# Optimization experiments

Hardware: AMD Instinct MI355X
Metric: run time of the kernel (lower is better)

## Reference

```python
import jax, jax.numpy as jnp
import numpy as np

EPS = 1e-5  # GraphNorm eps


def setup_inputs() -> dict:
    key = jax.random.key(0)
    ks = jax.random.split(key, 8)
    B, N, D, L = 8, 2048, 128, 3
    return {
        "instance": jax.random.uniform(ks[0], (B, N, 2), jnp.float32),
        "Wn": jax.random.normal(ks[1], (D, 2), jnp.float32) * 0.5,
        "bn": jnp.zeros((D,), jnp.float32),
        "Wg": jax.random.normal(ks[2], (L, D, D), jnp.float32) / np.sqrt(D).astype(np.float32),
        "bg": jnp.zeros((L, D), jnp.float32),
        "gn_w": jnp.ones((D,), jnp.float32),
        "gn_b": jnp.zeros((D,), jnp.float32),
        "gn_a": jnp.ones((D,), jnp.float32),
    }


def reference(instance, Wn, bn, Wg, bg, gn_w, gn_b, gn_a):
    # instance: [B, N, 2] city coordinates. Graph is complete, so the PyG
    # edge-list GCN over all (i != j) pairs + self-loops is exactly a dense
    # symmetric-normalized adjacency matmul per graph.
    B, N, _ = instance.shape
    # pairwise Euclidean distances (cdist), safe sqrt to keep diagonal exact 0
    sq = jnp.sum(instance * instance, axis=-1)                      # [B, N]
    d2 = sq[:, :, None] + sq[:, None, :] - 2.0 * jnp.einsum(
        'bnd,bmd->bnm', instance, instance)                          # [B, N, N]
    pos = d2 > 0
    dist = jnp.where(pos, jnp.sqrt(jnp.where(pos, d2, 1.0)), 0.0)    # [B, N, N]
    # GCN edge weights = distances, self-loops added with weight 1.0
    A = dist + jnp.eye(N, dtype=dist.dtype)
    deg = jnp.sum(A, axis=-1)                                        # [B, N]
    dinv = jax.lax.rsqrt(deg)
    An = dinv[:, :, None] * A * dinv[:, None, :]                     # D^-1/2 A D^-1/2

    h = jnp.einsum('bne,de->bnd', instance, Wn) + bn                 # proj_node
    for l in range(Wg.shape[0]):
        # GCNConv: aggregate normalized messages of lin(x), then bias
        hw = jnp.einsum('bnm,bmd->bnd', An, jnp.einsum('bnd,ed->bne', h, Wg[l])) + bg[l]
        h = jnp.tanh(hw) + h                                         # activation + residual
        # GraphNorm (shared params across layers): per-graph, per-feature stats
        mean = jnp.mean(h, axis=1, keepdims=True)                    # [B, 1, D]
        sub = h - gn_a * mean
        var = jnp.mean(sub * sub, axis=1, keepdims=True)
        h = gn_w * sub * jax.lax.rsqrt(var + EPS) + gn_b
    return h  # [B, N, D] (unbatch+stack of equal-size graphs)
```

## Files before the change

### kernel.cpp

```cpp
#include <hip/hip_runtime.h>
#include <hip/hip_bf16.h>
#include <math.h>

#define BB 8
#define NN 2048
#define DD 128
#define LL 3
#define GN_EPS 1e-5f

typedef __attribute__((ext_vector_type(8))) short bf16x8;
typedef __attribute__((ext_vector_type(4))) float f32x4;
typedef __attribute__((ext_vector_type(8))) unsigned short u16x8;

#define FSQRT(x) __builtin_amdgcn_sqrtf(x)

__device__ __forceinline__ unsigned short f2bf(float f) {
    union { float f; unsigned u; } v; v.f = f;
    return (unsigned short)((v.u + 0x8000u) >> 16);
}

__device__ __forceinline__ float fast_tanh(float x) {
    float e = __expf(-2.0f * fabsf(x));
    float t = (1.0f - e) * __builtin_amdgcn_rcpf(1.0f + e);
    return copysignf(t, x);
}

__device__ __forceinline__ void stats_sc(float ps, float pq, float a, float w_,
                                         float b_, float& s, float& c) {
    const float inv_n = 1.0f / (float)NN;
    float mean = ps * inv_n;
    float msq  = pq * inv_n;
    float var  = msq - mean * mean * a * (2.0f - a);
    float rstd = rsqrtf(var + GN_EPS);
    s = w_ * rstd;
    c = b_ - s * (a * mean);
}


__global__ __launch_bounds__(256)
void prep_wg(const float* __restrict__ Wg, const float* __restrict__ Wn,
             const float* __restrict__ bn, unsigned short* __restrict__ wgf,
             float* __restrict__ weff, float* __restrict__ beff)
{
    const int f = blockIdx.x * 256 + threadIdx.x;
    const int l  = f >> 14;
    const int r  = f & 16383;
    const int dp = r >> 7;
    const int e  = r & 127;
    const int dpt = dp >> 4, ll = dp & 15;
    const int kc  = e >> 5,  eo = e & 31;
    wgf[((((l * 8 + dpt) * 4 + kc) * 16 + ll) << 5) + eo] = f2bf(Wg[f]);

    if (blockIdx.x == 0 && threadIdx.x < 128) {
        const int ee = threadIdx.x;
        float a0 = 0.f, a1 = 0.f, cc = 0.f;
        for (int d = 0; d < 128; ++d) {
            const float wv = Wg[ee * 128 + d];
            a0 = fmaf(wv, Wn[d * 2 + 0], a0);
            a1 = fmaf(wv, Wn[d * 2 + 1], a1);
            cc = fmaf(wv, bn[d], cc);
        }
        weff[ee * 2 + 0] = a0;
        weff[ee * 2 + 1] = a1;
        beff[ee] = cc;
    }
}

__global__ __launch_bounds__(256)
void gen_pack(const float* __restrict__ inst, const float* __restrict__ Wn,
              const float* __restrict__ bn, const float* __restrict__ weff,
              const float* __restrict__ beff,
              float* __restrict__ dinv, float* __restrict__ h,
              unsigned short* __restrict__ tp,
              float* __restrict__ psum, float* __restrict__ psq)
{
    __shared__ float cs[NN * 2];
    __shared__ float part[4][16];
    const int b     = blockIdx.x & 7;
    const int ntile = blockIdx.x >> 3;
    const int n0    = ntile * 16;
    const int tid   = threadIdx.x;
    const int w     = tid >> 6;
    const int lane  = tid & 63;
    const int lq    = lane >> 4;
    const int ll    = lane & 15;

    const float* instb = inst + b * NN * 2;
    for (int i = tid; i < (NN * 2) / 4; i += 256)
        ((float4*)cs)[i] = ((const float4*)instb)[i];
    __syncthreads();

    const int n = n0 + ll;
    const float nx = cs[n * 2 + 0];
    const float ny = cs[n * 2 + 1];

    const int diagkcg = ntile >> 1;
    float rs = 0.f;
    for (int kc = 0; kc < 16; ++kc) {
        const int kcg = w * 16 + kc;
        const int mb  = kcg * 32 + lq * 8;
        const float* cp = &cs[mb * 2];
        float4 c01 = *(const float4*)(cp + 0);
        float4 c23 = *(const float4*)(cp + 4);
        float4 c45 = *(const float4*)(cp + 8);
        float4 c67 = *(const float4*)(cp + 12);
        float mxx[8] = { c01.x, c01.z, c23.x, c23.z, c45.x, c45.z, c67.x, c67.z };
        float myy[8] = { c01.y, c01.w, c23.y, c23.w, c45.y, c45.w, c67.y, c67.w };
        float dist[8];
        #pragma unroll
        for (int j = 0; j < 8; ++j) {
            float dx = nx - mxx[j];
            float dy = ny - myy[j];
            dist[j] = FSQRT(dx * dx + dy * dy);
        }
        if (kcg == diagkcg) {
            #pragma unroll
            for (int j = 0; j < 8; ++j)
                if (mb + j == n) dist[j] = 1.0f;
        }
        #pragma unroll
        for (int j = 0; j < 8; ++j) rs += dist[j];
    }

    rs += __shfl_xor(rs, 16);
    rs += __shfl_xor(rs, 32);
    if (lq == 0) part[w][ll] = rs;
    __syncthreads();
    if (tid < 16)
        dinv[b * NN + n0 + tid] = rsqrtf(part[0][tid] + part[1][tid] +
                                         part[2][tid] + part[3][tid]);

    {
        const int d  = tid & 127;
        const int r0 = tid >> 7;
        const float w0 = Wn[d * 2 + 0];
        const float w1 = Wn[d * 2 + 1];
        const float bv = bn[d];
        const float we0 = weff[d * 2 + 0];
        const float we1 = weff[d * 2 + 1];
        const float be  = beff[d];
        const int kcg   = ntile >> 1;
        const int mbase = (ntile & 1) * 16;
        const int dt    = d >> 4;
        const int lld   = d & 15;
        unsigned short* tpd =
            tp + (((size_t)(b * 64 + kcg) * 8 + dt) * 64 + lld) * 8;
        #pragma unroll
        for (int r = r0; r < 16; r += 2) {
            const float x0 = cs[(n0 + r) * 2 + 0];
            const float x1 = cs[(n0 + r) * 2 + 1];
            h[((size_t)b * NN + n0 + r) * DD + d] = fmaf(x0, w0, fmaf(x1, w1, bv));
            const float dv = rsqrtf(part[0][r] + part[1][r] + part[2][r] + part[3][r]);
            const int mloc = mbase + r;
            const int lqa  = mloc >> 3;
            const int j    = mloc & 7;
            tpd[(size_t)lqa * 128 + j] = f2bf(dv * fmaf(x0, we0, fmaf(x1, we1, be)));
        }
    }
    if (blockIdx.x == 0) {
        for (int i = tid; i < LL * BB * DD; i += 256) { psum[i] = 0.f; psq[i] = 0.f; }
    }
}

template <bool HP>
__global__ __launch_bounds__(256)
void lin_mfma(const float* __restrict__ h, const unsigned short* __restrict__ wgf_l,
              const float* __restrict__ dinv,
              const float* __restrict__ psumP, const float* __restrict__ psqP,
              const float* __restrict__ ga, const float* __restrict__ gw,
              const float* __restrict__ gb, unsigned short* __restrict__ tp)
{
    __shared__ float sL[DD], cL[DD];
    const int tid  = threadIdx.x;
    const int b    = blockIdx.x & 7;
    const int tile = blockIdx.x >> 3;
    const int row0 = b * NN + tile * 32;
    const int w    = tid >> 6;
    const int lane = tid & 63;
    const int lq   = lane >> 4;
    const int ll   = lane & 15;

    if (tid < DD) {
        float s = 1.0f, c = 0.0f;
        if (HP)
            stats_sc(psumP[b * DD + tid], psqP[b * DD + tid],
                     ga[tid], gw[tid], gb[tid], s, c);
        sL[tid] = s; cL[tid] = c;
    }
    __syncthreads();

    bf16x8 aw[2][4];
    #pragma unroll
    for (int mt = 0; mt < 2; ++mt) {
        const int dpt = 2 * w + mt;
        #pragma unroll
        for (int kc = 0; kc < 4; ++kc)
            aw[mt][kc] = *(const bf16x8*)&wgf_l[(((dpt * 4 + kc) * 16 + ll) << 5) + lq * 8];
    }

    bf16x8 bh[2][4];
    #pragma unroll
    for (int nt = 0; nt < 2; ++nt) {
        const float* hrow = h + (size_t)(row0 + nt * 16 + ll) * DD;
        #pragma unroll
        for (int kc = 0; kc < 4; ++kc) {
            float4 h0 = *(const float4*)&hrow[kc * 32 + lq * 8];
            float4 h1 = *(const float4*)&hrow[kc * 32 + lq * 8 + 4];
            const int e0 = kc * 32 + lq * 8;
            bf16x8 p;
            p[0] = (short)f2bf(fmaf(sL[e0 + 0], h0.x, cL[e0 + 0]));
            p[1] = (short)f2bf(fmaf(sL[e0 + 1], h0.y, cL[e0 + 1]));
            p[2] = (short)f2bf(fmaf(sL[e0 + 2], h0.z, cL[e0 + 2]));
            p[3] = (short)f2bf(fmaf(sL[e0 + 3], h0.w, cL[e0 + 3]));
            p[4] = (short)f2bf(fmaf(sL[e0 + 4], h1.x, cL[e0 + 4]));
            p[5] = (short)f2bf(fmaf(sL[e0 + 5], h1.y, cL[e0 + 5]));
            p[6] = (short)f2bf(fmaf(sL[e0 + 6], h1.z, cL[e0 + 6]));
            p[7] = (short)f2bf(fmaf(sL[e0 + 7], h1.w, cL[e0 + 7]));
            bh[nt][kc] = p;
        }
    }

    f32x4 acc[2][2];
    #pragma unroll
    for (int i = 0; i < 2; ++i)
        #pragma unroll
        for (int j = 0; j < 2; ++j) acc[i][j] = (f32x4)0.0f;

    #pragma unroll
    for (int kc = 0; kc < 4; ++kc)
        #pragma unroll
        for (int nt = 0; nt < 2; ++nt)
            #pragma unroll
            for (int mt = 0; mt < 2; ++mt)
                acc[nt][mt] = __builtin_amdgcn_mfma_f32_16x16x32_bf16(
                    bh[nt][kc], aw[mt][kc], acc[nt][mt], 0, 0, 0);

    #pragma unroll
    for (int nt = 0; nt < 2; ++nt) {
        const int mloc0 = nt * 16 + lq * 4;
        const int lq_a  = mloc0 >> 3;
        const int j0    = mloc0 & 7;
        float4 di4 = *(const float4*)&dinv[row0 + mloc0];
        #pragma unroll
        for (int mt = 0; mt < 2; ++mt) {
            const int dt = 2 * w + mt;
            ushort4 pk;
            pk.x = f2bf(acc[nt][mt][0] * di4.x);
            pk.y = f2bf(acc[nt][mt][1] * di4.y);
            pk.z = f2bf(acc[nt][mt][2] * di4.z);
            pk.w = f2bf(acc[nt][mt][3] * di4.w);
            *(ushort4*)&tp[((size_t)((b * 64 + tile) * 8 + dt) * 64 + lq_a * 16 + ll) * 8 + j0] = pk;
        }
    }
}

template <bool HP>
__global__ __launch_bounds__(256, 2)
void agg_mfma(const float* __restrict__ inst, const unsigned short* __restrict__ tp,
              const float* __restrict__ dinv, const float* __restrict__ bg_l,
              const float* __restrict__ psumP, const float* __restrict__ psqP,
              const float* __restrict__ ga, const float* __restrict__ gw,
              const float* __restrict__ gb,
              float* __restrict__ h, float* __restrict__ psum, float* __restrict__ psq)
{
    __shared__ float cs[NN * 2];
    __shared__ __align__(16) char plane[2][32768];
    const int b    = blockIdx.x & 7;
    const int t2   = blockIdx.x >> 3;
    const int n0   = t2 * 32;
    const int tid  = threadIdx.x;
    const int w    = tid >> 6;
    const int lane = tid & 63;
    const int lq   = lane >> 4;
    const int ll   = lane & 15;

    const float* instb = inst + b * NN * 2;
    for (int i = tid; i < (NN * 2) / 4; i += 256)
        ((float4*)cs)[i] = ((const float4*)instb)[i];

    const unsigned short* tpb = tp + ((size_t)b * 64 * 8) * 512 + lane * 8;

    f32x4 acc[2][2];
    acc[0][0] = (f32x4)0.0f; acc[0][1] = (f32x4)0.0f;
    acc[1][0] = (f32x4)0.0f; acc[1][1] = (f32x4)0.0f;

    bf16x8 fbA0[4], fbA1[4], fbB0[4], fbB1[4];

    __syncthreads();

    const int   nr0 = n0 + ll;
    const int   nr1 = n0 + 16 + ll;
    const float nx0 = cs[nr0 * 2 + 0], ny0 = cs[nr0 * 2 + 1];
    const float nx1 = cs[nr1 * 2 + 0], ny1 = cs[nr1 * 2 + 1];

#define LOADB_INTO(B0, B1, KK) { \
        _Pragma("unroll") \
        for (int s_ = 0; s_ < 4; ++s_) { \
            B0[s_] = *(const bf16x8*)(tpb + (size_t)(((KK) * 4 + s_) * 8 + 2 * w + 0) * 512); \
            B1[s_] = *(const bf16x8*)(tpb + (size_t)(((KK) * 4 + s_) * 8 + 2 * w + 1) * 512); \
        } \
    }

#define GENQ(PL, PH, Q) { \
        const int kcg_ = (PH) * 16 + w * 4 + (Q); \
        const int mb_  = kcg_ * 32 + lq * 8; \
        const float* cp_ = &cs[mb_ * 2]; \
        float4 c01 = *(const float4*)(cp_ + 0); \
        float4 c23 = *(const float4*)(cp_ + 4); \
        float4 c45 = *(const float4*)(cp_ + 8); \
        float4 c67 = *(const float4*)(cp_ + 12); \
        float mxx[8] = { c01.x, c01.z, c23.x, c23.z, c45.x, c45.z, c67.x, c67.z }; \
        float myy[8] = { c01.y, c01.w, c23.y, c23.w, c45.y, c45.w, c67.y, c67.w }; \
        float dv0[8], dv1[8]; \
        _Pragma("unroll") \
        for (int j = 0; j < 8; ++j) { \
            float dx0 = nx0 - mxx[j], dy0 = ny0 - myy[j]; \
            dv0[j] = FSQRT(dx0 * dx0 + dy0 * dy0); \
            float dx1 = nx1 - mxx[j], dy1 = ny1 - myy[j]; \
            dv1[j] = FSQRT(dx1 * dx1 + dy1 * dy1); \
        } \
        if (kcg_ == t2) {    \
            _Pragma("unroll") \
            for (int j = 0; j < 8; ++j) { \
                if (mb_ + j == nr0) dv0[j] = 1.0f; \
                if (mb_ + j == nr1) dv1[j] = 1.0f; \
            } \
        } \
        u16x8 pk0, pk1; \
        _Pragma("unroll") \
        for (int j = 0; j < 8; ++j) { pk0[j] = f2bf(dv0[j]); pk1[j] = f2bf(dv1[j]); } \
        *(u16x8*)(plane[PL] + (w * 8 + 0 + (Q)) * 1024 + lane * 16) = pk0; \
        *(u16x8*)(plane[PL] + (w * 8 + 4 + (Q)) * 1024 + lane * 16) = pk1; \
    }

#define STEP(PL, I, C0, C1, DOLOAD, N0, N1, KN) { \
        bf16x8 af[2][4]; \
        _Pragma("unroll") \
        for (int nt = 0; nt < 2; ++nt) \
            _Pragma("unroll") \
            for (int s = 0; s < 4; ++s) \
                af[nt][s] = *(const bf16x8*)(plane[PL] + (((I) * 8 + nt * 4 + s) * 1024) + lane * 16); \
        if (DOLOAD) LOADB_INTO(N0, N1, KN) \
        _Pragma("unroll") \
        for (int s = 0; s < 4; ++s) \
            _Pragma("unroll") \
            for (int nt = 0; nt < 2; ++nt) { \
                acc[nt][0] = __builtin_amdgcn_mfma_f32_16x16x32_bf16(C0[s], af[nt][s], acc[nt][0], 0, 0, 0); \
                acc[nt][1] = __builtin_amdgcn_mfma_f32_16x16x32_bf16(C1[s], af[nt][s], acc[nt][1], 0, 0, 0); \
            } \
    }

    GENQ(0, 0, 0) GENQ(0, 0, 1) GENQ(0, 0, 2) GENQ(0, 0, 3)
    LOADB_INTO(fbA0, fbA1, 0)
    __syncthreads();

    STEP(0, 0, fbA0, fbA1, true, fbB0, fbB1, 1)   GENQ(1, 1, 0)
    STEP(0, 1, fbB0, fbB1, true, fbA0, fbA1, 2)   GENQ(1, 1, 1)
    STEP(0, 2, fbA0, fbA1, true, fbB0, fbB1, 3)   GENQ(1, 1, 2)
    STEP(0, 3, fbB0, fbB1, true, fbA0, fbA1, 4)   GENQ(1, 1, 3)
    __syncthreads();

    STEP(1, 0, fbA0, fbA1, true, fbB0, fbB1, 5)   GENQ(0, 2, 0)
    STEP(1, 1, fbB0, fbB1, true, fbA0, fbA1, 6)   GENQ(0, 2, 1)
    STEP(1, 2, fbA0, fbA1, true, fbB0, fbB1, 7)   GENQ(0, 2, 2)
    STEP(1, 3, fbB0, fbB1, true, fbA0, fbA1, 8)   GENQ(0, 2, 3)
    __syncthreads();

    STEP(0, 0, fbA0, fbA1, true, fbB0, fbB1, 9)   GENQ(1, 3, 0)
    STEP(0, 1, fbB0, fbB1, true, fbA0, fbA1, 10)  GENQ(1, 3, 1)
    STEP(0, 2, fbA0, fbA1, true, fbB0, fbB1, 11)  GENQ(1, 3, 2)
    STEP(0, 3, fbB0, fbB1, true, fbA0, fbA1, 12)  GENQ(1, 3, 3)
    __syncthreads();

    STEP(1, 0, fbA0, fbA1, true,  fbB0, fbB1, 13)
    STEP(1, 1, fbB0, fbB1, true,  fbA0, fbA1, 14)
    STEP(1, 2, fbA0, fbA1, true,  fbB0, fbB1, 15)
    STEP(1, 3, fbB0, fbB1, false, fbA0, fbA1, 0)

#undef STEP
#undef GENQ
#undef LOADB_INTO

    const float di0 = dinv[b * NN + n0 + ll];
    const float di1 = dinv[b * NN + n0 + 16 + ll];
    #pragma unroll
    for (int dtl = 0; dtl < 2; ++dtl) {
        const int d0 = (2 * w + dtl) * 16 + lq * 4;
        float4 bg4 = *(const float4*)&bg_l[d0];
        float sres[4] = {1.f, 1.f, 1.f, 1.f}, cres[4] = {0.f, 0.f, 0.f, 0.f};
        if (HP) {
            float4 ps4 = *(const float4*)&psumP[b * DD + d0];
            float4 pq4 = *(const float4*)&psqP[b * DD + d0];
            float4 ga4 = *(const float4*)&ga[d0];
            float4 gw4 = *(const float4*)&gw[d0];
            float4 gb4 = *(const float4*)&gb[d0];
            stats_sc(ps4.x, pq4.x, ga4.x, gw4.x, gb4.x, sres[0], cres[0]);
            stats_sc(ps4.y, pq4.y, ga4.y, gw4.y, gb4.y, sres[1], cres[1]);
            stats_sc(ps4.z, pq4.z, ga4.z, gw4.z, gb4.z, sres[2], cres[2]);
            stats_sc(ps4.w, pq4.w, ga4.w, gw4.w, gb4.w, sres[3], cres[3]);
        }
        float hs[4] = {0.f, 0.f, 0.f, 0.f}, hq[4] = {0.f, 0.f, 0.f, 0.f};
        #pragma unroll
        for (int nt = 0; nt < 2; ++nt) {
            const int n = n0 + nt * 16 + ll;
            const float di = nt ? di1 : di0;
            size_t idx = ((size_t)b * NN + n) * DD + d0;
            float4 hv = *(const float4*)&h[idx];
            float outv[4];
            #pragma unroll
            for (int r = 0; r < 4; ++r) {
                float pre = di * acc[nt][dtl][r] + (&bg4.x)[r];
                outv[r] = fast_tanh(pre) + fmaf(sres[r], (&hv.x)[r], cres[r]);
                hs[r] += outv[r];
                hq[r] += outv[r] * outv[r];
            }
            float4 ov = { outv[0], outv[1], outv[2], outv[3] };
            *(float4*)&h[idx] = ov;
        }

        #pragma unroll
        for (int off = 1; off < 16; off <<= 1) {
            #pragma unroll
            for (int r = 0; r < 4; ++r) {
                hs[r] += __shfl_xor(hs[r], off);
                hq[r] += __shfl_xor(hq[r], off);
            }
        }
        if (ll == 0) {
            #pragma unroll
            for (int r = 0; r < 4; ++r) {
                atomicAdd(&psum[b * DD + d0 + r], hs[r]);
                atomicAdd(&psq[b * DD + d0 + r], hq[r]);
            }
        }
    }
}

__global__ __launch_bounds__(256)
void apply_kernel(const float* __restrict__ h,
                  const float* __restrict__ psum2, const float* __restrict__ psq2,
                  const float* __restrict__ ga, const float* __restrict__ gw,
                  const float* __restrict__ gb, float* __restrict__ dst)
{
    const int i4 = blockIdx.x * 256 + threadIdx.x;
    const int dg = (i4 & 31) * 4;
    const int b  = i4 >> 16;
    float4 hv = ((const float4*)h)[i4];
    float o[4];
    #pragma unroll
    for (int j = 0; j < 4; ++j) {
        const int d = dg + j;
        float s, c;
        stats_sc(psum2[b * DD + d], psq2[b * DD + d], ga[d], gw[d], gb[d], s, c);
        o[j] = fmaf(s, (&hv.x)[j], c);
    }
    float4 ov = { o[0], o[1], o[2], o[3] };
    ((float4*)dst)[i4] = ov;
}

extern "C" void kernel_launch(void* const* d_in, const int* in_sizes, int n_in,
                              void* d_out, int out_size, void* d_ws, size_t ws_size,
                              hipStream_t stream)
{
    const float* inst = (const float*)d_in[0];
    const float* Wn   = (const float*)d_in[1];
    const float* bn   = (const float*)d_in[2];
    const float* Wg   = (const float*)d_in[3];
    const float* bg   = (const float*)d_in[4];
    const float* gw   = (const float*)d_in[5];
    const float* gb   = (const float*)d_in[6];
    const float* ga   = (const float*)d_in[7];
    float* out = (float*)d_out;

    float* ws   = (float*)d_ws;
    float* dinv = ws;
    float* h    = dinv + BB * NN;
    float* psum = h + (size_t)BB * NN * DD;
    float* psq  = psum + LL * BB * DD;
    float* weff = psq + LL * BB * DD;
    float* beff = weff + 2 * DD;
    unsigned short* wgf = (unsigned short*)(beff + DD);
    unsigned short* tp  = wgf + LL * DD * DD;

    prep_wg<<<(LL * DD * DD) / 256, 256, 0, stream>>>(Wg, Wn, bn, wgf, weff, beff);
    gen_pack<<<1024, 256, 0, stream>>>(inst, Wn, bn, weff, beff, dinv, h, tp, psum, psq);

    agg_mfma<false><<<512, 256, 0, stream>>>(
        inst, tp, dinv, bg + 0 * DD, nullptr, nullptr, ga, gw, gb, h, psum, psq);

    for (int l = 1; l < LL; ++l) {
        const unsigned short* wgl = wgf + (size_t)l * DD * DD;
        const float* psP = psum + (size_t)(l - 1) * BB * DD;
        const float* pqP = psq  + (size_t)(l - 1) * BB * DD;
        float* psL = psum + (size_t)l * BB * DD;
        float* pqL = psq  + (size_t)l * BB * DD;
        lin_mfma<true><<<(BB * NN) / 32, 256, 0, stream>>>(
            h, wgl, dinv, psP, pqP, ga, gw, gb, tp);
        agg_mfma<true><<<512, 256, 0, stream>>>(
            inst, tp, dinv, bg + l * DD, psP, pqP, ga, gw, gb, h, psL, pqL);
    }
    apply_kernel<<<(BB * NN * DD / 4) / 256, 256, 0, stream>>>(
        h, psum + 2 * BB * DD, psq + 2 * BB * DD, ga, gw, gb, out);
}
```

Before: 176.4 us.

## Split K across waves in aggregation kernel with LDS cross-wave reduction

The aggregation kernel previously had each wave own two output D-tiles over the full K range. Distance tiles were shared between waves through double-buffered LDS planes with barriers. Now each wave takes a quarter of the K range for all eight D-tiles. It computes its distance fragments directly in registers and never exchanges them through LDS, which removes the per-phase barriers. The partial accumulators are then reduced across waves through a 64KB LDS buffer. In exchange each wave recomputes no distances but needs 16 accumulator vectors plus 16 B-fragment registers, so register pressure rises and occupancy under launch_bounds(256,2) may suffer.

```diff
diff --git a/kernel.cpp b/kernel.cpp
--- a/kernel.cpp
+++ b/kernel.cpp
@@ -264,7 +264,7 @@
               float* __restrict__ h, float* __restrict__ psum, float* __restrict__ psq)
 {
     __shared__ float cs[NN * 2];
-    __shared__ __align__(16) char plane[2][32768];
+    __shared__ __align__(16) char red[65536];
     const int b    = blockIdx.x & 7;
     const int t2   = blockIdx.x >> 3;
     const int n0   = t2 * 32;
@@ -280,11 +280,13 @@
 
     const unsigned short* tpb = tp + ((size_t)b * 64 * 8) * 512 + lane * 8;
 
-    f32x4 acc[2][2];
-    acc[0][0] = (f32x4)0.0f; acc[0][1] = (f32x4)0.0f;
-    acc[1][0] = (f32x4)0.0f; acc[1][1] = (f32x4)0.0f;
-
-    bf16x8 fbA0[4], fbA1[4], fbB0[4], fbB1[4];
+    f32x4 acc[2][8];
+    #pragma unroll
+    for (int nt = 0; nt < 2; ++nt)
+        #pragma unroll
+        for (int dt = 0; dt < 8; ++dt) acc[nt][dt] = (f32x4)0.0f;
+
+    bf16x8 fbE[8], fbO[8];
 
     __syncthreads();
 
@@ -293,16 +295,16 @@
     const float nx0 = cs[nr0 * 2 + 0], ny0 = cs[nr0 * 2 + 1];
     const float nx1 = cs[nr1 * 2 + 0], ny1 = cs[nr1 * 2 + 1];
 
-#define LOADB_INTO(B0, B1, KK) { \
+    const int kcg0 = w * 16;
+
+#define LOADB(DST, KCG) { \
         _Pragma("unroll") \
-        for (int s_ = 0; s_ < 4; ++s_) { \
-            B0[s_] = *(const bf16x8*)(tpb + (size_t)(((KK) * 4 + s_) * 8 + 2 * w + 0) * 512); \
-            B1[s_] = *(const bf16x8*)(tpb + (size_t)(((KK) * 4 + s_) * 8 + 2 * w + 1) * 512); \
-        } \
-    }
-
-#define GENQ(PL, PH, Q) { \
-        const int kcg_ = (PH) * 16 + w * 4 + (Q); \
+        for (int dt_ = 0; dt_ < 8; ++dt_) \
+            DST[dt_] = *(const bf16x8*)(tpb + (size_t)((KCG) * 8 + dt_) * 512); \
+    }
+
+#define STEPK(KC, CUR, NXT, DOLOAD) { \
+        const int kcg_ = kcg0 + (KC); \
         const int mb_  = kcg_ * 32 + lq * 8; \
         const float* cp_ = &cs[mb_ * 2]; \
         float4 c01 = *(const float4*)(cp_ + 0); \
@@ -326,60 +328,60 @@
                 if (mb_ + j == nr1) dv1[j] = 1.0f; \
             } \
         } \
-        u16x8 pk0, pk1; \
+        bf16x8 af0, af1; \
         _Pragma("unroll") \
-        for (int j = 0; j < 8; ++j) { pk0[j] = f2bf(dv0[j]); pk1[j] = f2bf(dv1[j]); } \
-        *(u16x8*)(plane[PL] + (w * 8 + 0 + (Q)) * 1024 + lane * 16) = pk0; \
-        *(u16x8*)(plane[PL] + (w * 8 + 4 + (Q)) * 1024 + lane * 16) = pk1; \
-    }
-
-#define STEP(PL, I, C0, C1, DOLOAD, N0, N1, KN) { \
-        bf16x8 af[2][4]; \
+        for (int j = 0; j < 8; ++j) { \
+            af0[j] = (short)f2bf(dv0[j]); \
+            af1[j] = (short)f2bf(dv1[j]); \
+        } \
+        if (DOLOAD) LOADB(NXT, kcg_ + 1) \
         _Pragma("unroll") \
-        for (int nt = 0; nt < 2; ++nt) \
-            _Pragma("unroll") \
-            for (int s = 0; s < 4; ++s) \
-                af[nt][s] = *(const bf16x8*)(plane[PL] + (((I) * 8 + nt * 4 + s) * 1024) + lane * 16); \
-        if (DOLOAD) LOADB_INTO(N0, N1, KN) \
-        _Pragma("unroll") \
-        for (int s = 0; s < 4; ++s) \
-            _Pragma("unroll") \
-            for (int nt = 0; nt < 2; ++nt) { \
-                acc[nt][0] = __builtin_amdgcn_mfma_f32_16x16x32_bf16(C0[s], af[nt][s], acc[nt][0], 0, 0, 0); \
-                acc[nt][1] = __builtin_amdgcn_mfma_f32_16x16x32_bf16(C1[s], af[nt][s], acc[nt][1], 0, 0, 0); \
-            } \
-    }
-
-    GENQ(0, 0, 0) GENQ(0, 0, 1) GENQ(0, 0, 2) GENQ(0, 0, 3)
-    LOADB_INTO(fbA0, fbA1, 0)
+        for (int dt_ = 0; dt_ < 8; ++dt_) { \
+            acc[0][dt_] = __builtin_amdgcn_mfma_f32_16x16x32_bf16(CUR[dt_], af0, acc[0][dt_], 0, 0, 0); \
+            acc[1][dt_] = __builtin_amdgcn_mfma_f32_16x16x32_bf16(CUR[dt_], af1, acc[1][dt_], 0, 0, 0); \
+        } \
+    }
+
+    LOADB(fbE, kcg0)
+    STEPK(0,  fbE, fbO, true)
+    STEPK(1,  fbO, fbE, true)
+    STEPK(2,  fbE, fbO, true)
+    STEPK(3,  fbO, fbE, true)
+    STEPK(4,  fbE, fbO, true)
+    STEPK(5,  fbO, fbE, true)
+    STEPK(6,  fbE, fbO, true)
+    STEPK(7,  fbO, fbE, true)
+    STEPK(8,  fbE, fbO, true)
+    STEPK(9,  fbO, fbE, true)
+    STEPK(10, fbE, fbO, true)
+    STEPK(11, fbO, fbE, true)
+    STEPK(12, fbE, fbO, true)
+    STEPK(13, fbO, fbE, true)
+    STEPK(14, fbE, fbO, true)
+    STEPK(15, fbO, fbE, false)
+#undef STEPK
+#undef LOADB
+
+    #pragma unroll
+    for (int nt = 0; nt < 2; ++nt)
+        #pragma unroll
+        for (int dt = 0; dt < 8; ++dt)
+            *(f32x4*)(red + (((dt * 2 + nt) * 4 + w) * 1024) + lane * 16) = acc[nt][dt];
     __syncthreads();
 
-    STEP(0, 0, fbA0, fbA1, true, fbB0, fbB1, 1)   GENQ(1, 1, 0)
-    STEP(0, 1, fbB0, fbB1, true, fbA0, fbA1, 2)   GENQ(1, 1, 1)
-    STEP(0, 2, fbA0, fbA1, true, fbB0, fbB1, 3)   GENQ(1, 1, 2)
-    STEP(0, 3, fbB0, fbB1, true, fbA0, fbA1, 4)   GENQ(1, 1, 3)
-    __syncthreads();
-
-    STEP(1, 0, fbA0, fbA1, true, fbB0, fbB1, 5)   GENQ(0, 2, 0)
-    STEP(1, 1, fbB0, fbB1, true, fbA0, fbA1, 6)   GENQ(0, 2, 1)
-    STEP(1, 2, fbA0, fbA1, true, fbB0, fbB1, 7)   GENQ(0, 2, 2)
-    STEP(1, 3, fbB0, fbB1, true, fbA0, fbA1, 8)   GENQ(0, 2, 3)
-    __syncthreads();
-
-    STEP(0, 0, fbA0, fbA1, true, fbB0, fbB1, 9)   GENQ(1, 3, 0)
-    STEP(0, 1, fbB0, fbB1, true, fbA0, fbA1, 10)  GENQ(1, 3, 1)
-    STEP(0, 2, fbA0, fbA1, true, fbB0, fbB1, 11)  GENQ(1, 3, 2)
-    STEP(0, 3, fbB0, fbB1, true, fbA0, fbA1, 12)  GENQ(1, 3, 3)
-    __syncthreads();
-
-    STEP(1, 0, fbA0, fbA1, true,  fbB0, fbB1, 13)
-    STEP(1, 1, fbB0, fbB1, true,  fbA0, fbA1, 14)
-    STEP(1, 2, fbA0, fbA1, true,  fbB0, fbB1, 15)
-    STEP(1, 3, fbB0, fbB1, false, fbA0, fbA1, 0)
-
-#undef STEP
-#undef GENQ
-#undef LOADB_INTO
+    f32x4 accs[2][2];
+    #pragma unroll
+    for (int dtl = 0; dtl < 2; ++dtl) {
+        const int dt = 2 * w + dtl;
+        #pragma unroll
+        for (int nt = 0; nt < 2; ++nt) {
+            f32x4 r0 = *(const f32x4*)(red + (((dt * 2 + nt) * 4 + 0) * 1024) + lane * 16);
+            f32x4 r1 = *(const f32x4*)(red + (((dt * 2 + nt) * 4 + 1) * 1024) + lane * 16);
+            f32x4 r2 = *(const f32x4*)(red + (((dt * 2 + nt) * 4 + 2) * 1024) + lane * 16);
+            f32x4 r3 = *(const f32x4*)(red + (((dt * 2 + nt) * 4 + 3) * 1024) + lane * 16);
+            accs[nt][dtl] = ((r0 + r1) + r2) + r3;
+        }
+    }
 
     const float di0 = dinv[b * NN + n0 + ll];
     const float di1 = dinv[b * NN + n0 + 16 + ll];
@@ -409,7 +411,7 @@
             float outv[4];
             #pragma unroll
             for (int r = 0; r < 4; ++r) {
-                float pre = di * acc[nt][dtl][r] + (&bg4.x)[r];
+                float pre = di * accs[nt][dtl][r] + (&bg4.x)[r];
                 outv[r] = fast_tanh(pre) + fmaf(sres[r], (&hv.x)[r], cres[r]);
                 hs[r] += outv[r];
                 hq[r] += outv[r] * outv[r];
```

After: 173.6 us. About the same (-1.6%).
